# Optimization experiments

Measured on AMD Instinct MI355X. Metric: run time of the kernel, lower is better.

The kernel has to match this reference:

```python
import jax, jax.numpy as jnp
import numpy as np


def _conv_valid(x, w, b):
    # x: NHWC, w: HWIO
    y = jax.lax.conv_general_dilated(x, w, window_strides=(1, 1), padding='VALID',
                                     dimension_numbers=('NHWC', 'HWIO', 'NHWC'))
    return y + b


def _maxpool2(x):
    return jax.lax.reduce_window(x, -jnp.inf, jax.lax.max,
                                 (1, 2, 2, 1), (1, 2, 2, 1), 'VALID')


def setup_inputs() -> dict:
    key = jax.random.key(0)
    ks = jax.random.split(key, 12)
    B, H, W = 128, 256, 256
    FLAT = 61 * 61 * 32  # 256 ->(conv5 valid) 252 ->(pool) 126 ->(conv5) 122 ->(pool) 61
    x = jax.random.uniform(ks[0], (B, H, W, 1), dtype=jnp.float32)
    conv1_w = jax.random.normal(ks[1], (5, 5, 1, 14), dtype=jnp.float32) * 0.05
    conv1_b = jnp.zeros((14,), jnp.float32)
    conv2_w = jax.random.normal(ks[2], (5, 5, 14, 32), dtype=jnp.float32) * 0.05
    conv2_b = jnp.zeros((32,), jnp.float32)
    d1_w = jax.random.normal(ks[3], (FLAT, 120), dtype=jnp.float32) * 0.005
    d1_b = jnp.zeros((120,), jnp.float32)
    d2_w = jax.random.normal(ks[4], (120, 84), dtype=jnp.float32) * 0.05
    d2_b = jnp.zeros((84,), jnp.float32)
    # last dense: zero-init kernel + identity affine bias in the original;
    # use a tiny random kernel so the warp is a nontrivial near-identity affine.
    d3_w = jax.random.normal(ks[5], (84, 6), dtype=jnp.float32) * 1e-3
    d3_b = jnp.array([1, 0, 0, 0, 1, 0], dtype=jnp.float32)
    out_w = jax.random.normal(ks[6], (1, 1, 1, 1), dtype=jnp.float32)
    out_b = jnp.zeros((1,), jnp.float32)
    return {'x': x, 'conv1_w': conv1_w, 'conv1_b': conv1_b,
            'conv2_w': conv2_w, 'conv2_b': conv2_b,
            'd1_w': d1_w, 'd1_b': d1_b, 'd2_w': d2_w, 'd2_b': d2_b,
            'd3_w': d3_w, 'd3_b': d3_b, 'out_w': out_w, 'out_b': out_b}


def reference(x, conv1_w, conv1_b, conv2_w, conv2_b,
              d1_w, d1_b, d2_w, d2_b, d3_w, d3_b, out_w, out_b):
    B, H, W, _ = x.shape
    # --- localization network (dropout is inference-mode identity) ---
    h = _maxpool2(jax.nn.relu(_conv_valid(x, conv1_w, conv1_b)))
    h = _maxpool2(jax.nn.relu(_conv_valid(h, conv2_w, conv2_b)))
    h = h.reshape(B, -1)
    h = jax.nn.relu(h @ d1_w + d1_b)
    h = jax.nn.relu(h @ d2_w + d2_b)
    theta = (h @ d3_w + d3_b).reshape(B, 2, 3)  # affine params
    # --- normalized homogeneous meshgrid (xy indexing, row-major flatten) ---
    xs = (jnp.arange(W, dtype=jnp.float32) / W - 0.5) * 2.0
    ys = (jnp.arange(H, dtype=jnp.float32) / H - 0.5) * 2.0
    gx, gy = jnp.meshgrid(xs, ys)  # [H, W]
    grid = jnp.stack([gx.ravel(), gy.ravel(), jnp.ones(H * W, jnp.float32)], axis=-1)  # [HW, 3]
    # --- transform grids into pixel coords ---
    rep = jnp.einsum('bij,pj->bpi', theta, grid)            # [B, HW, 2]
    rep = (rep + 1.0) * 0.5 * jnp.array([W, H], jnp.float32)
    px, py = rep[..., 0], rep[..., 1]                        # [B, HW]
    # --- four clipped neighbors ---
    x1 = jnp.clip(jnp.floor(px).astype(jnp.int32), 0, W - 1)
    x2 = jnp.clip(jnp.floor(px).astype(jnp.int32) + 1, 0, W - 1)
    y1 = jnp.clip(jnp.floor(py).astype(jnp.int32), 0, H - 1)
    y2 = jnp.clip(jnp.floor(py).astype(jnp.int32) + 1, 0, H - 1)
    img = x[..., 0].reshape(B, H * W)  # C == 1
    gather = lambda yi, xi: jnp.take_along_axis(img, yi * W + xi, axis=1)
    p11 = gather(y1, x1)  # pixel at (x1, y1)
    p12 = gather(y2, x1)  # (x1, y2)
    p21 = gather(y1, x2)  # (x2, y1)
    p22 = gather(y2, x2)  # (x2, y2)
    # --- bilinear weights (use clipped neighbor coords, as in the original) ---
    wx1 = x2.astype(jnp.float32) - px
    wx2 = px - x1.astype(jnp.float32)
    wy1 = y2.astype(jnp.float32) - py
    wy2 = py - y1.astype(jnp.float32)
    r = wx1 * (wy1 * p11 + wy2 * p12) + wx2 * (wy1 * p21 + wy2 * p22)  # [B, HW]
    r = r.reshape(B, H, W, 1)
    # --- 1x1 conv + sigmoid output head ---
    out = jax.nn.sigmoid(r * out_w[0, 0, 0, 0] + out_b[0])
    return out
```

## Files before the change

### kernel.cpp

```cpp
#include <hip/hip_runtime.h>

#define TH_OFF   0ull
#define H1_OFF   4096ull
#define P1_OFF   65536ull
#define PART_OFF 65536ull
#define P2_OFF   113930240ull

__global__ __launch_bounds__(256) void k_c1(const float* __restrict__ x,
        const float* __restrict__ w1, const float* __restrict__ b1,
        float* __restrict__ p1)
{
    __shared__ float s_in[36*36];
    __shared__ float s_w[350];
    __shared__ float s_b[14];
    const int b   = blockIdx.z;
    const int ty0 = blockIdx.y * 16, tx0 = blockIdx.x * 16;
    const int tid = threadIdx.x;
    for (int i = tid; i < 36*36; i += 256) {
        int r = i / 36, c = i % 36;
        int gy = 2*ty0 + r, gx = 2*tx0 + c;
        float v = 0.f;
        if (gy < 256 && gx < 256) v = x[(long)(b*256 + gy)*256 + gx];
        s_in[i] = v;
    }
    for (int i = tid; i < 350; i += 256) s_w[i] = w1[i];
    if (tid < 14) s_b[tid] = b1[tid];
    __syncthreads();

    const int py = tid >> 4, px = tid & 15;
    float a0[14], a1[14], a2[14], a3[14];
    #pragma unroll
    for (int c = 0; c < 14; ++c) { a0[c]=0.f; a1[c]=0.f; a2[c]=0.f; a3[c]=0.f; }
    const int iy = 2*py, ix = 2*px;
    #pragma unroll
    for (int ky = 0; ky < 5; ++ky) {
      #pragma unroll
      for (int kx = 0; kx < 5; ++kx) {
        float wv[14];
        #pragma unroll
        for (int c = 0; c < 14; ++c) wv[c] = s_w[(ky*5+kx)*14 + c];
        const float* ip = &s_in[(iy+ky)*36 + ix + kx];
        float v00 = ip[0],  v01 = ip[1];
        float v10 = ip[36], v11 = ip[37];
        #pragma unroll
        for (int c = 0; c < 14; ++c) {
            a0[c] = fmaf(v00, wv[c], a0[c]);
            a1[c] = fmaf(v01, wv[c], a1[c]);
            a2[c] = fmaf(v10, wv[c], a2[c]);
            a3[c] = fmaf(v11, wv[c], a3[c]);
        }
      }
    }
    const int oy = ty0 + py, ox = tx0 + px;
    if (oy < 126 && ox < 126) {
        float* op = &p1[((long)(b*126 + oy)*126 + ox)*14];
        #pragma unroll
        for (int c = 0; c < 14; ++c) {
            float bb = s_b[c];
            float m = fmaxf(__fadd_rn(a0[c], bb), 0.f);
            m = fmaxf(m, fmaxf(__fadd_rn(a1[c], bb), 0.f));
            m = fmaxf(m, fmaxf(__fadd_rn(a2[c], bb), 0.f));
            m = fmaxf(m, fmaxf(__fadd_rn(a3[c], bb), 0.f));
            op[c] = m;
        }
    }
}

__global__ __launch_bounds__(256) void k_c2(const float* __restrict__ p1,
        const float* __restrict__ w2, const float* __restrict__ b2,
        float* __restrict__ p2)
{
    __shared__ float s_w[25*14*32];
    __shared__ float s_in[20*20*15];
    const int b   = blockIdx.z;
    const int ty0 = blockIdx.y * 8, tx0 = blockIdx.x * 8;
    const int tid = threadIdx.x;
    for (int i = tid; i < 11200; i += 256) s_w[i] = w2[i];
    for (int i = tid; i < 5600; i += 256) {
        int ic = i % 14, rem = i / 14;
        int cc = rem % 20, r = rem / 20;
        int gy = 2*ty0 + r, gx = 2*tx0 + cc;
        float v = 0.f;
        if (gy < 126 && gx < 126) v = p1[((long)(b*126 + gy)*126 + gx)*14 + ic];
        s_in[(r*20 + cc)*15 + ic] = v;
    }
    __syncthreads();

    const int pos = tid & 63, cg = tid >> 6;
    const int ppy = pos >> 3, ppx = pos & 7;
    const int ocb = cg * 8;
    float acc[4][8];
    #pragma unroll
    for (int j = 0; j < 4; ++j)
      #pragma unroll
      for (int c = 0; c < 8; ++c) acc[j][c] = 0.f;

    const int by = 2*ppy, bx = 2*ppx;
    for (int ky = 0; ky < 5; ++ky) {
      for (int kx = 0; kx < 5; ++kx) {
        const float* r0 = &s_in[((by + ky)*20 + bx + kx)*15];
        const float* r1 = &s_in[((by + 1 + ky)*20 + bx + kx)*15];
        const float* wp0 = &s_w[((ky*5 + kx)*14)*32 + ocb];
        #pragma unroll
        for (int ic = 0; ic < 14; ++ic) {
            const float* wp = wp0 + ic*32;
            float4 wA = *reinterpret_cast<const float4*>(wp);
            float4 wB = *reinterpret_cast<const float4*>(wp + 4);
            float wv[8] = {wA.x,wA.y,wA.z,wA.w,wB.x,wB.y,wB.z,wB.w};
            float v00 = r0[ic],      v01 = r0[15 + ic];
            float v10 = r1[ic],      v11 = r1[15 + ic];
            #pragma unroll
            for (int c = 0; c < 8; ++c) {
                acc[0][c] = fmaf(v00, wv[c], acc[0][c]);
                acc[1][c] = fmaf(v01, wv[c], acc[1][c]);
                acc[2][c] = fmaf(v10, wv[c], acc[2][c]);
                acc[3][c] = fmaf(v11, wv[c], acc[3][c]);
            }
        }
      }
    }
    const int oy = ty0 + ppy, ox = tx0 + ppx;
    if (oy < 61 && ox < 61) {
        float* op = &p2[(long)b*119072 + (long)(oy*61 + ox)*32 + ocb];
        #pragma unroll
        for (int c = 0; c < 8; ++c) {
            float bb = b2[ocb + c];
            float m = fmaxf(__fadd_rn(acc[0][c], bb), 0.f);
            m = fmaxf(m, fmaxf(__fadd_rn(acc[1][c], bb), 0.f));
            m = fmaxf(m, fmaxf(__fadd_rn(acc[2][c], bb), 0.f));
            m = fmaxf(m, fmaxf(__fadd_rn(acc[3][c], bb), 0.f));
            op[c] = m;
        }
    }
}

__global__ __launch_bounds__(128) void k_d1a(const float* __restrict__ p2,
        const float* __restrict__ w, float* __restrict__ part)
{
    const int n = threadIdx.x;
    const int panel = blockIdx.x;
    const int b0 = blockIdx.y * 32;
    if (n >= 120) return;
    const int kp = panel * 384;
    const int ke = (kp + 384 < 119072) ? kp + 384 : 119072;
    const float* a0 = p2 + (long)b0 * 119072;
    float p[32];
    #pragma unroll
    for (int i = 0; i < 32; ++i) p[i] = 0.f;
    for (int k = kp; k < ke; ++k) {
        float wv = w[(long)k * 120 + n];
        #pragma unroll
        for (int i = 0; i < 32; ++i)
            p[i] = fmaf(a0[(long)i * 119072 + k], wv, p[i]);
    }
    #pragma unroll
    for (int i = 0; i < 32; ++i)
        part[((long)panel * 128 + b0 + i) * 120 + n] = p[i];
}

__global__ __launch_bounds__(128) void k_d1b(const float* __restrict__ part,
        float* __restrict__ h1)
{
    const int b = blockIdx.x, n = threadIdx.x;
    if (n >= 120) return;
    float h = 0.f;
    for (int p = 0; p < 311; ++p)
        h = __fadd_rn(h, part[((long)p * 128 + b) * 120 + n]);
    h1[b * 120 + n] = h;
}

__global__ __launch_bounds__(128) void k_head(const float* __restrict__ h1,
        const float* __restrict__ d1b, const float* __restrict__ d2w,
        const float* __restrict__ d2b, const float* __restrict__ d3w,
        const float* __restrict__ d3b, float* __restrict__ theta)
{
    __shared__ float s1[120], s2[84];
    const int b = blockIdx.x, t = threadIdx.x;
    if (t < 120) s1[t] = fmaxf(__fadd_rn(h1[b * 120 + t], d1b[t]), 0.f);
    __syncthreads();
    if (t < 84) {
        float a = 0.f;
        for (int k = 0; k < 120; ++k) a = fmaf(s1[k], d2w[k * 84 + t], a);
        s2[t] = fmaxf(__fadd_rn(a, d2b[t]), 0.f);
    }
    __syncthreads();
    if (t < 6) {
        float a = 0.f;
        for (int k = 0; k < 84; ++k) a = fmaf(s2[k], d3w[k * 6 + t], a);
        theta[b * 6 + t] = __fadd_rn(a, d3b[t]);
    }
}

__global__ __launch_bounds__(256) void k_sample(const float* __restrict__ x,
        const float* __restrict__ theta, const float* __restrict__ ow,
        const float* __restrict__ ob, float* __restrict__ out)
{
    const int idx = blockIdx.x * 256 + threadIdx.x;
    const int b   = idx >> 16;
    const int pix = idx & 65535;
    const int yy  = pix >> 8, xx = pix & 255;
    const float gx = __fadd_rn((float)xx * (1.f / 128.f), -1.f);
    const float gy = __fadd_rn((float)yy * (1.f / 128.f), -1.f);
    const float* th = &theta[b * 6];
    float rx = __fmul_rn(th[0], gx);
    rx = fmaf(th[1], gy, rx);
    rx = __fadd_rn(rx, th[2]);
    float ry = __fmul_rn(th[3], gx);
    ry = fmaf(th[4], gy, ry);
    ry = __fadd_rn(ry, th[5]);
    const float px = __fmul_rn(__fmul_rn(__fadd_rn(rx, 1.f), 0.5f), 256.f);
    const float py = __fmul_rn(__fmul_rn(__fadd_rn(ry, 1.f), 0.5f), 256.f);
    int x1 = (int)floorf(px), y1 = (int)floorf(py);
    int x2 = x1 + 1,  y2 = y1 + 1;
    x1 = min(max(x1, 0), 255); x2 = min(max(x2, 0), 255);
    y1 = min(max(y1, 0), 255); y2 = min(max(y2, 0), 255);
    const float* img = x + (long)b * 65536;
    const float p11 = img[y1 * 256 + x1];
    const float p12 = img[y2 * 256 + x1];
    const float p21 = img[y1 * 256 + x2];
    const float p22 = img[y2 * 256 + x2];
    const float wx1 = __fsub_rn((float)x2, px);
    const float wx2 = __fsub_rn(px, (float)x1);
    const float wy1 = __fsub_rn((float)y2, py);
    const float wy2 = __fsub_rn(py, (float)y1);
    const float sa = __fadd_rn(__fmul_rn(wy1, p11), __fmul_rn(wy2, p12));
    const float sb = __fadd_rn(__fmul_rn(wy1, p21), __fmul_rn(wy2, p22));
    const float r  = __fadd_rn(__fmul_rn(wx1, sa), __fmul_rn(wx2, sb));
    const float o  = __fadd_rn(__fmul_rn(r, ow[0]), ob[0]);
    out[idx] = 1.f / (1.f + expf(-o));
}

extern "C" void kernel_launch(void* const* d_in, const int* in_sizes, int n_in,
                              void* d_out, int out_size, void* d_ws, size_t ws_size,
                              hipStream_t stream)
{
    const float* x   = (const float*)d_in[0];
    const float* c1w = (const float*)d_in[1];
    const float* c1b = (const float*)d_in[2];
    const float* c2w = (const float*)d_in[3];
    const float* c2b = (const float*)d_in[4];
    const float* d1w = (const float*)d_in[5];
    const float* d1b = (const float*)d_in[6];
    const float* d2w = (const float*)d_in[7];
    const float* d2b = (const float*)d_in[8];
    const float* d3w = (const float*)d_in[9];
    const float* d3b = (const float*)d_in[10];
    const float* ow  = (const float*)d_in[11];
    const float* ob  = (const float*)d_in[12];

    char*  ws   = (char*)d_ws;
    float* th   = (float*)(ws + TH_OFF);
    float* h1   = (float*)(ws + H1_OFF);
    float* p1   = (float*)(ws + P1_OFF);
    float* part = (float*)(ws + PART_OFF);
    float* p2   = (float*)(ws + P2_OFF);

    k_c1    <<<dim3(8, 8, 128),  256, 0, stream>>>(x, c1w, c1b, p1);
    k_c2    <<<dim3(8, 8, 128),  256, 0, stream>>>(p1, c2w, c2b, p2);
    k_d1a   <<<dim3(311, 4),     128, 0, stream>>>(p2, d1w, part);
    k_d1b   <<<dim3(128),        128, 0, stream>>>(part, h1);
    k_head  <<<dim3(128),        128, 0, stream>>>(h1, d1b, d2w, d2b, d3w, d3b, th);
    k_sample<<<dim3(32768),      256, 0, stream>>>(x, th, ow, ob, (float*)d_out);
}
```

Baseline: 1.248 ms.

## Restructure conv2 into larger tiles with row-wise register reuse and shuffle pooling

Conv2 now has each block compute a 16x16 pooled tile with 1024 threads. Each thread computes one pre-pool row pair of outputs for 16 channels, and the input is stored as [row][ic][col] so that float2 loads are reused across the sliding kx window. The vertical max-pool pair is combined with a lane shuffle instead of per-thread 2x2 accumulators. The aim is fewer LDS loads per FMA and less halo overhead. The costs are higher register pressure at 1024-thread blocks, a larger shared footprint (about 71 KB for input plus 44 KB for weights) that cuts occupancy, and half the lanes idle during stores.

```diff
diff --git a/kernel.cpp b/kernel.cpp
--- a/kernel.cpp
+++ b/kernel.cpp
@@ -66,71 +66,86 @@
     }
 }
 
-__global__ __launch_bounds__(256) void k_c2(const float* __restrict__ p1,
+#define C2_BLOCK(KX, VL, VR)                                        \
+  { const int kb = (ky*5 + (KX))*14;                                \
+    _Pragma("unroll")                                               \
+    for (int ic = 0; ic < 14; ++ic) {                               \
+      const float* wp = &s_w[(kb + ic)*32 + ocb];                   \
+      float4 wA = *reinterpret_cast<const float4*>(wp);             \
+      float4 wB = *reinterpret_cast<const float4*>(wp + 4);         \
+      float4 wC = *reinterpret_cast<const float4*>(wp + 8);         \
+      float4 wD = *reinterpret_cast<const float4*>(wp + 12);        \
+      float wv[16] = {wA.x,wA.y,wA.z,wA.w, wB.x,wB.y,wB.z,wB.w,     \
+                      wC.x,wC.y,wC.z,wC.w, wD.x,wD.y,wD.z,wD.w};    \
+      float vl = (VL), vr = (VR);                                   \
+      _Pragma("unroll")                                             \
+      for (int c = 0; c < 16; ++c) {                                \
+        accL[c] = fmaf(vl, wv[c], accL[c]);                         \
+        accR[c] = fmaf(vr, wv[c], accR[c]);                         \
+      } } }
+
+__global__ __launch_bounds__(1024) void k_c2(const float* __restrict__ p1,
         const float* __restrict__ w2, const float* __restrict__ b2,
         float* __restrict__ p2)
 {
     __shared__ float s_w[25*14*32];
-    __shared__ float s_in[20*20*15];
+    __shared__ float s_in[36*14*38];
     const int b   = blockIdx.z;
-    const int ty0 = blockIdx.y * 8, tx0 = blockIdx.x * 8;
+    const int ty0 = blockIdx.y * 16, tx0 = blockIdx.x * 16;
     const int tid = threadIdx.x;
-    for (int i = tid; i < 11200; i += 256) s_w[i] = w2[i];
-    for (int i = tid; i < 5600; i += 256) {
+
+    for (int i = tid; i < 11200; i += 1024) s_w[i] = w2[i];
+    for (int i = tid; i < 36*36*14; i += 1024) {
         int ic = i % 14, rem = i / 14;
-        int cc = rem % 20, r = rem / 20;
+        int cc = rem % 36, r = rem / 36;
         int gy = 2*ty0 + r, gx = 2*tx0 + cc;
         float v = 0.f;
         if (gy < 126 && gx < 126) v = p1[((long)(b*126 + gy)*126 + gx)*14 + ic];
-        s_in[(r*20 + cc)*15 + ic] = v;
-    }
-    __syncthreads();
-
-    const int pos = tid & 63, cg = tid >> 6;
-    const int ppy = pos >> 3, ppx = pos & 7;
-    const int ocb = cg * 8;
-    float acc[4][8];
-    #pragma unroll
-    for (int j = 0; j < 4; ++j)
-      #pragma unroll
-      for (int c = 0; c < 8; ++c) acc[j][c] = 0.f;
-
-    const int by = 2*ppy, bx = 2*ppx;
+        s_in[(r*14 + ic)*38 + cc] = v;
+    }
+    __syncthreads();
+
+    const int cg  = tid >> 9;
+    const int t   = tid & 511;
+    const int py  = t >> 4;
+    const int ppx = t & 15;
+    const int ocb = cg * 16;
+    const int bx  = 2 * ppx;
+
+    float accL[16], accR[16];
+    #pragma unroll
+    for (int c = 0; c < 16; ++c) { accL[c] = 0.f; accR[c] = 0.f; }
+
     for (int ky = 0; ky < 5; ++ky) {
-      for (int kx = 0; kx < 5; ++kx) {
-        const float* r0 = &s_in[((by + ky)*20 + bx + kx)*15];
-        const float* r1 = &s_in[((by + 1 + ky)*20 + bx + kx)*15];
-        const float* wp0 = &s_w[((ky*5 + kx)*14)*32 + ocb];
-        #pragma unroll
-        for (int ic = 0; ic < 14; ++ic) {
-            const float* wp = wp0 + ic*32;
-            float4 wA = *reinterpret_cast<const float4*>(wp);
-            float4 wB = *reinterpret_cast<const float4*>(wp + 4);
-            float wv[8] = {wA.x,wA.y,wA.z,wA.w,wB.x,wB.y,wB.z,wB.w};
-            float v00 = r0[ic],      v01 = r0[15 + ic];
-            float v10 = r1[ic],      v11 = r1[15 + ic];
-            #pragma unroll
-            for (int c = 0; c < 8; ++c) {
-                acc[0][c] = fmaf(v00, wv[c], acc[0][c]);
-                acc[1][c] = fmaf(v01, wv[c], acc[1][c]);
-                acc[2][c] = fmaf(v10, wv[c], acc[2][c]);
-                acc[3][c] = fmaf(v11, wv[c], acc[3][c]);
-            }
-        }
-      }
-    }
-    const int oy = ty0 + ppy, ox = tx0 + ppx;
-    if (oy < 61 && ox < 61) {
-        float* op = &p2[(long)b*119072 + (long)(oy*61 + ox)*32 + ocb];
-        #pragma unroll
-        for (int c = 0; c < 8; ++c) {
-            float bb = b2[ocb + c];
-            float m = fmaxf(__fadd_rn(acc[0][c], bb), 0.f);
-            m = fmaxf(m, fmaxf(__fadd_rn(acc[1][c], bb), 0.f));
-            m = fmaxf(m, fmaxf(__fadd_rn(acc[2][c], bb), 0.f));
-            m = fmaxf(m, fmaxf(__fadd_rn(acc[3][c], bb), 0.f));
-            op[c] = m;
-        }
+        const float* rp = &s_in[((py + ky)*14)*38 + bx];
+        float2 X[14], Y[14];
+        #pragma unroll
+        for (int ic = 0; ic < 14; ++ic)
+            X[ic] = *reinterpret_cast<const float2*>(rp + ic*38);
+        #pragma unroll
+        for (int ic = 0; ic < 14; ++ic)
+            Y[ic] = *reinterpret_cast<const float2*>(rp + ic*38 + 2);
+        C2_BLOCK(0, X[ic].x, X[ic].y)
+        C2_BLOCK(1, X[ic].y, Y[ic].x)
+        C2_BLOCK(2, Y[ic].x, Y[ic].y)
+        #pragma unroll
+        for (int ic = 0; ic < 14; ++ic)
+            X[ic] = *reinterpret_cast<const float2*>(rp + ic*38 + 4);
+        C2_BLOCK(3, Y[ic].y, X[ic].x)
+        C2_BLOCK(4, X[ic].x, X[ic].y)
+    }
+
+    const int prow = ty0 + (py >> 1);
+    const int pcol = tx0 + ppx;
+    const bool wr = ((py & 1) == 0) && prow < 61 && pcol < 61;
+    float* op = &p2[(long)b*119072 + (long)(prow*61 + pcol)*32 + ocb];
+    #pragma unroll
+    for (int c = 0; c < 16; ++c) {
+        float bb = b2[ocb + c];
+        float m0 = fmaxf(__fadd_rn(accL[c], bb), 0.f);
+        m0 = fmaxf(m0, fmaxf(__fadd_rn(accR[c], bb), 0.f));
+        float m1 = __shfl_xor(m0, 16, 64);
+        if (wr) op[c] = fmaxf(m0, m1);
     }
 }
 
@@ -255,10 +270,10 @@
     float* part = (float*)(ws + PART_OFF);
     float* p2   = (float*)(ws + P2_OFF);
 
-    k_c1    <<<dim3(8, 8, 128),  256, 0, stream>>>(x, c1w, c1b, p1);
-    k_c2    <<<dim3(8, 8, 128),  256, 0, stream>>>(p1, c2w, c2b, p2);
-    k_d1a   <<<dim3(311, 4),     128, 0, stream>>>(p2, d1w, part);
-    k_d1b   <<<dim3(128),        128, 0, stream>>>(part, h1);
-    k_head  <<<dim3(128),        128, 0, stream>>>(h1, d1b, d2w, d2b, d3w, d3b, th);
-    k_sample<<<dim3(32768),      256, 0, stream>>>(x, th, ow, ob, (float*)d_out);
-}
+    k_c1    <<<dim3(8, 8, 128),  256,  0, stream>>>(x, c1w, c1b, p1);
+    k_c2    <<<dim3(4, 4, 128),  1024, 0, stream>>>(p1, c2w, c2b, p2);
+    k_d1a   <<<dim3(311, 4),     128,  0, stream>>>(p2, d1w, part);
+    k_d1b   <<<dim3(128),        128,  0, stream>>>(part, h1);
+    k_head  <<<dim3(128),        128,  0, stream>>>(h1, d1b, d2w, d2b, d3w, d3b, th);
+    k_sample<<<dim3(32768),      256,  0, stream>>>(x, th, ow, ob, (float*)d_out);
+}
```

Measured after the change: 1.282 ms. 2.7% more time.
